# Performance work log

Hardware: AMD Instinct MI355X
Metric: run time of the kernel (lower is better)

The kernel has to match this reference:

```python
import jax, jax.numpy as jnp
import numpy as np
import math

H, Dh, S = 8, 64, 3          # heads, dim per head, samples factor
B, T, N, K = 2, 12, 512, 16  # batch, time, nodes, local-adj width
F = H * Dh                   # features = 512
SN = int(S * math.log2(N))   # Sampled_Nodes = 27
EPS = 1e-5


def setup_inputs() -> dict:
    key = jax.random.key(0)
    ks = jax.random.split(key, 22)
    sc = 1.0 / math.sqrt(F)
    W = lambda k: jax.random.normal(k, (F, F), jnp.float32) * sc
    bb = lambda k: jax.random.normal(k, (F,), jnp.float32) * 0.01
    return {
        "x": jax.random.normal(ks[0], (B, T, N, F), jnp.float32),
        "spa_eigvalue": jax.random.normal(ks[1], (F,), jnp.float32) * 0.1,
        "spa_eigvec": jax.random.normal(ks[2], (N, F), jnp.float32) * 0.1,
        "tem_eigvalue": jax.random.normal(ks[3], (F,), jnp.float32) * 0.1,
        "tem_eigvec": jax.random.normal(ks[4], (N, F), jnp.float32) * 0.1,
        "localadj": jax.random.randint(ks[5], (N, K), 0, N),
        "Wq": W(ks[6]), "bq": bb(ks[7]),
        "Wk": W(ks[8]), "bk": bb(ks[9]),
        "Wv": W(ks[10]), "bv": bb(ks[11]),
        "Wo": W(ks[12]), "bo": bb(ks[13]),
        "w_proj": jax.random.normal(ks[14], (K,), jnp.float32) / math.sqrt(K),
        "b_proj": jax.random.normal(ks[15], (), jnp.float32) * 0.01,
        "gamma": jnp.ones((F,), jnp.float32),
        "beta": jnp.zeros((F,), jnp.float32),
        "W1": W(ks[16]), "b1": bb(ks[17]),
        "W2": W(ks[18]), "b2": bb(ks[19]),
    }


def _lin(v, Wm, bv):  # torch nn.Linear: y = x @ W^T + b, W is [out, in]
    return jnp.einsum('...i,oi->...o', v, Wm) + bv


def _ln(v, g=None, b=None):  # LayerNorm over last dim, eps=1e-5
    mu = jnp.mean(v, -1, keepdims=True)
    var = jnp.var(v, -1, keepdims=True)
    y = (v - mu) * jax.lax.rsqrt(var + EPS)
    return y * g + b if g is not None else y


def reference(x, spa_eigvalue, spa_eigvec, tem_eigvalue, tem_eigvec, localadj,
              Wq, bq, Wk, bk, Wv, bv, Wo, bo, w_proj, b_proj,
              gamma, beta, W1, b1, W2, b2):
    # eigvec @ diag(eigval) == row-wise scaling
    x_ = x + (spa_eigvec * spa_eigvalue + tem_eigvec * tem_eigvalue)
    to_heads = lambda v: v.reshape(B, T, N, H, Dh).transpose(3, 0, 1, 2, 4)  # [H,B,T,N,Dh]
    Qh = to_heads(_lin(x_, Wq, bq))
    Kh = to_heads(_lin(x_, Wk, bk))
    Vh = to_heads(_lin(x_, Wv, bv))
    # local-adjacency K sampling: [H,B,T,N,K,Dh]
    Ks = Kh[:, :, :, localadj, :]
    qks = jnp.einsum('hbtnd,hbtnkd->hbtnk', Qh, Ks)
    # importance score per query node via learned projection over K neighbors
    M = jnp.einsum('hbtnk,k->hbtn', qks, w_proj) + b_proj
    _, m_top = jax.lax.top_k(M, SN)                              # [H,B,T,SN]
    Qr = jnp.take_along_axis(Qh, m_top[..., None], axis=3)       # [H,B,T,SN,Dh]
    scores = jnp.einsum('hbtsd,hbtnd->hbtsn', Qr, Kh) / math.sqrt(Dh)
    attn = jax.nn.softmax(scores, axis=-1)                       # [H,B,T,SN,N]
    cp = jnp.argmax(attn, axis=-2)                               # best sampled query per key node [H,B,T,N]
    val = jnp.einsum('hbtsn,hbtnd->hbtsd', attn, Vh)             # [H,B,T,SN,Dh]
    out = jnp.take_along_axis(val, cp[..., None], axis=3)        # [H,B,T,N,Dh]
    out = out.transpose(1, 2, 3, 0, 4).reshape(B, T, N, F)       # merge heads
    v = _ln(_lin(out, Wo, bo), gamma, beta)
    h = jax.nn.relu(_lin(v, W1, b1))
    h = _lin(h, W2, b2) + v
    return _ln(h)
```

## Files before the change

### kernel.cpp

```cpp
#include <hip/hip_runtime.h>
#include <math.h>

#define H_    8
#define DH    64
#define NN    512
#define KADJ  16
#define FF    512
#define BTOT  24
#define ROWS  12288
#define SN_   27
#define EPS_  1e-5f

typedef short short8 __attribute__((ext_vector_type(8)));
typedef float f32x4  __attribute__((ext_vector_type(4)));

__device__ __forceinline__ ushort f2bf(float x) {
    uint u = __float_as_uint(x);
    u += 0x7FFFu + ((u >> 16) & 1u);
    return (ushort)(u >> 16);
}
__device__ __forceinline__ float bf2f(ushort h) {
    return __uint_as_float(((uint)h) << 16);
}
__device__ __forceinline__ void pack_hilo(float4 a, float4 b, short8& hi, short8& lo) {
    float v[8] = {a.x, a.y, a.z, a.w, b.x, b.y, b.z, b.w};
    #pragma unroll
    for (int j = 0; j < 8; ++j) {
        ushort h = f2bf(v[j]);
        hi[j] = (short)h;
        lo[j] = (short)f2bf(v[j] - bf2f(h));
    }
}

__device__ __forceinline__ void gload_lds16(const ushort* g, ushort* l) {
    __builtin_amdgcn_global_load_lds(
        (const __attribute__((address_space(1))) unsigned int*)g,
        (__attribute__((address_space(3))) unsigned int*)l,
        16, 0, 0);
}

__global__ __launch_bounds__(256) void add_pos_bf16(
    const float* __restrict__ x,
    const float* __restrict__ spa_val, const float* __restrict__ spa_vec,
    const float* __restrict__ tem_val, const float* __restrict__ tem_vec,
    ushort* __restrict__ xh, ushort* __restrict__ xl)
{
    int i = blockIdx.x * 256 + threadIdx.x;
    int f4  = i & 127;
    int row = i >> 7;
    int n   = row & (NN - 1);

    float4 xv = reinterpret_cast<const float4*>(x)[i];
    float4 sv = reinterpret_cast<const float4*>(spa_vec)[n * 128 + f4];
    float4 tv = reinterpret_cast<const float4*>(tem_vec)[n * 128 + f4];
    float4 se = reinterpret_cast<const float4*>(spa_val)[f4];
    float4 te = reinterpret_cast<const float4*>(tem_val)[f4];
    float r0 = xv.x + sv.x * se.x + tv.x * te.x;
    float r1 = xv.y + sv.y * se.y + tv.y * te.y;
    float r2 = xv.z + sv.z * se.z + tv.z * te.z;
    float r3 = xv.w + sv.w * se.w + tv.w * te.w;
    ushort h0 = f2bf(r0), h1 = f2bf(r1), h2 = f2bf(r2), h3 = f2bf(r3);
    reinterpret_cast<ushort4*>(xh)[i] = make_ushort4(h0, h1, h2, h3);
    reinterpret_cast<ushort4*>(xl)[i] = make_ushort4(
        f2bf(r0 - bf2f(h0)), f2bf(r1 - bf2f(h1)),
        f2bf(r2 - bf2f(h2)), f2bf(r3 - bf2f(h3)));
}

__global__ __launch_bounds__(256) void wconv_kernel(
    const float* __restrict__ w0, const float* __restrict__ w1,
    const float* __restrict__ w2, const float* __restrict__ w3,
    const float* __restrict__ w4, const float* __restrict__ w5,
    ushort* __restrict__ whi, ushort* __restrict__ wlo)
{
    const int wi = blockIdx.y;
    const float* W = wi == 0 ? w0 : wi == 1 ? w1 : wi == 2 ? w2 :
                     wi == 3 ? w3 : wi == 4 ? w4 : w5;
    int i = blockIdx.x * 256 + threadIdx.x;
    float4 v = reinterpret_cast<const float4*>(W)[i];
    ushort h0 = f2bf(v.x), h1 = f2bf(v.y), h2 = f2bf(v.z), h3 = f2bf(v.w);
    reinterpret_cast<ushort4*>(whi + (size_t)wi * 262144)[i] =
        make_ushort4(h0, h1, h2, h3);
    if (wi < 2) {
        reinterpret_cast<ushort4*>(wlo + (size_t)wi * 262144)[i] =
            make_ushort4(f2bf(v.x - bf2f(h0)), f2bf(v.y - bf2f(h1)),
                         f2bf(v.z - bf2f(h2)), f2bf(v.w - bf2f(h3)));
    }
}

#define GBM 64
#define GBN 128

template <int SPLIT, int EPI, int OUTBF>
__global__ __launch_bounds__(256, 2) void gemm_mfma2(
    const ushort* __restrict__ Ah, const ushort* __restrict__ Al,
    const ushort* __restrict__ Wh, const ushort* __restrict__ Wl,
    const float* __restrict__ bias, const float* __restrict__ addsrc,
    float* __restrict__ Cf, ushort* __restrict__ Cb)
{
    __shared__ ushort sA[GBM * 64];
    __shared__ ushort sB[GBN * 64];

    const int nx  = gridDim.x >> 3;
    const int bid = blockIdx.x;
    const int lt  = (bid & 7) * nx + (bid >> 3);
    const int rowBase = (lt >> 2) * GBM;
    const int colBase = (lt & 3) * GBN;

    const int tid  = threadIdx.x;
    const int lane = tid & 63;
    const int wid  = tid >> 6;
    const int q    = lane >> 4;
    const int fr   = lane & 15;
    const int wm   = wid & 1;
    const int wn   = wid >> 1;

    const int kadv = SPLIT ? 32 : 64;
    const ushort* asrc[2];
    const ushort* bsrc[4];
    #pragma unroll
    for (int c = 0; c < 2; ++c) {
        const int p   = wid * 2048 + c * 1024 + lane * 16;
        const int row = p >> 7;
        const int ss  = ((p >> 4) & 7) ^ (row & 7);
        if (!SPLIT)
            asrc[c] = Ah + (size_t)(rowBase + row) * FF + ss * 8;
        else
            asrc[c] = (ss < 4)
                ? Ah + (size_t)(rowBase + row) * FF + ss * 8
                : Al + (size_t)(rowBase + row) * FF + (ss - 4) * 8;
    }
    #pragma unroll
    for (int c = 0; c < 4; ++c) {
        const int p   = wid * 4096 + c * 1024 + lane * 16;
        const int row = p >> 7;
        const int ss  = ((p >> 4) & 7) ^ (row & 7);
        if (!SPLIT)
            bsrc[c] = Wh + (size_t)(colBase + row) * FF + ss * 8;
        else
            bsrc[c] = (ss < 4)
                ? Wh + (size_t)(colBase + row) * FF + ss * 8
                : Wl + (size_t)(colBase + row) * FF + (ss - 4) * 8;
    }

    f32x4 acc[2][4];
    #pragma unroll
    for (int mi = 0; mi < 2; ++mi)
        #pragma unroll
        for (int ni = 0; ni < 4; ++ni) acc[mi][ni] = (f32x4){0.f, 0.f, 0.f, 0.f};

    const int NSTEP = SPLIT ? 16 : 8;
    const int swz = fr & 7;

    for (int step = 0; step < NSTEP; ++step) {
        #pragma unroll
        for (int c = 0; c < 2; ++c) {
            gload_lds16(asrc[c], &sA[wid * 1024 + c * 512]);
            asrc[c] += kadv;
        }
        #pragma unroll
        for (int c = 0; c < 4; ++c) {
            gload_lds16(bsrc[c], &sB[wid * 2048 + c * 512]);
            bsrc[c] += kadv;
        }
        __syncthreads();

        if (!SPLIT) {
            #pragma unroll
            for (int ksub = 0; ksub < 2; ++ksub) {
                const int kq = ksub * 4 + q;
                short8 af[2], bf[4];
                #pragma unroll
                for (int mi = 0; mi < 2; ++mi)
                    af[mi] = *(const short8*)&sA[(wm * 32 + mi * 16 + fr) * 64 +
                                                 ((kq ^ swz) << 3)];
                #pragma unroll
                for (int ni = 0; ni < 4; ++ni)
                    bf[ni] = *(const short8*)&sB[(wn * 64 + ni * 16 + fr) * 64 +
                                                 ((kq ^ swz) << 3)];
                #pragma unroll
                for (int mi = 0; mi < 2; ++mi)
                    #pragma unroll
                    for (int ni = 0; ni < 4; ++ni)
                        acc[mi][ni] = __builtin_amdgcn_mfma_f32_16x16x32_bf16(
                            af[mi], bf[ni], acc[mi][ni], 0, 0, 0);
            }
        } else {
            short8 ah[2], bh[4], t[4];
            #pragma unroll
            for (int mi = 0; mi < 2; ++mi)
                ah[mi] = *(const short8*)&sA[(wm * 32 + mi * 16 + fr) * 64 +
                                             ((q ^ swz) << 3)];
            #pragma unroll
            for (int ni = 0; ni < 4; ++ni)
                bh[ni] = *(const short8*)&sB[(wn * 64 + ni * 16 + fr) * 64 +
                                             ((q ^ swz) << 3)];
            #pragma unroll
            for (int mi = 0; mi < 2; ++mi)
                #pragma unroll
                for (int ni = 0; ni < 4; ++ni)
                    acc[mi][ni] = __builtin_amdgcn_mfma_f32_16x16x32_bf16(
                        ah[mi], bh[ni], acc[mi][ni], 0, 0, 0);
            #pragma unroll
            for (int ni = 0; ni < 4; ++ni)
                t[ni] = *(const short8*)&sB[(wn * 64 + ni * 16 + fr) * 64 +
                                            (((q + 4) ^ swz) << 3)];
            #pragma unroll
            for (int mi = 0; mi < 2; ++mi)
                #pragma unroll
                for (int ni = 0; ni < 4; ++ni)
                    acc[mi][ni] = __builtin_amdgcn_mfma_f32_16x16x32_bf16(
                        ah[mi], t[ni], acc[mi][ni], 0, 0, 0);
            #pragma unroll
            for (int mi = 0; mi < 2; ++mi)
                t[mi] = *(const short8*)&sA[(wm * 32 + mi * 16 + fr) * 64 +
                                            (((q + 4) ^ swz) << 3)];
            #pragma unroll
            for (int mi = 0; mi < 2; ++mi)
                #pragma unroll
                for (int ni = 0; ni < 4; ++ni)
                    acc[mi][ni] = __builtin_amdgcn_mfma_f32_16x16x32_bf16(
                        t[mi], bh[ni], acc[mi][ni], 0, 0, 0);
        }
        __syncthreads();
    }

    #pragma unroll
    for (int mi = 0; mi < 2; ++mi)
        #pragma unroll
        for (int ni = 0; ni < 4; ++ni) {
            const int col = colBase + wn * 64 + ni * 16 + fr;
            const float bcol = bias[col];
            #pragma unroll
            for (int r = 0; r < 4; ++r) {
                const int row = rowBase + wm * 32 + mi * 16 + q * 4 + r;
                float v = acc[mi][ni][r] + bcol;
                if (EPI == 1) v = fmaxf(v, 0.0f);
                if (EPI == 2) v += addsrc[(size_t)row * FF + col];
                if (OUTBF) Cb[(size_t)row * FF + col] = f2bf(v);
                else       Cf[(size_t)row * FF + col] = v;
            }
        }
}

__global__ __launch_bounds__(256) void qks_M_kernel(
    const float* __restrict__ Q, const float* __restrict__ K,
    const int* __restrict__ adj, const float* __restrict__ w_proj,
    const float* __restrict__ b_proj, float* __restrict__ Mout)
{
    const int w = blockIdx.x * 4 + (threadIdx.x >> 6);
    const int lane = threadIdx.x & 63;
    const int n   = w & (NN - 1);
    const int hbt = w >> 9;
    const int h   = hbt / BTOT;
    const int bt  = hbt % BTOT;

    float s = 0.0f;
    #pragma unroll
    for (int k = 0; k < KADJ; ++k) {
        const int j = adj[n * KADJ + k];
        s += w_proj[k] * K[((size_t)(bt * NN + j)) * FF + h * DH + lane];
    }
    float t = Q[((size_t)(bt * NN + n)) * FF + h * DH + lane] * s;
    #pragma unroll
    for (int o = 32; o; o >>= 1) t += __shfl_xor(t, o);
    if (lane == 0) Mout[(size_t)hbt * NN + n] = t + b_proj[0];
}

__global__ __launch_bounds__(64) void topk_kernel(
    const float* __restrict__ M, int* __restrict__ mtop)
{
    const int g = blockIdx.x;
    __shared__ float vals[NN];
    const int lane = threadIdx.x;
    for (int i = lane; i < NN; i += 64) vals[i] = M[(size_t)g * NN + i];
    __syncthreads();

    for (int s = 0; s < SN_; ++s) {
        float bv = -INFINITY;
        int bi = 1 << 30;
        for (int i = lane; i < NN; i += 64) {
            float v = vals[i];
            if (v > bv || (v == bv && i < bi)) { bv = v; bi = i; }
        }
        #pragma unroll
        for (int o = 32; o; o >>= 1) {
            float ov = __shfl_xor(bv, o);
            int   oi = __shfl_xor(bi, o);
            if (ov > bv || (ov == bv && oi < bi)) { bv = ov; bi = oi; }
        }
        if (lane == 0) {
            mtop[g * SN_ + s] = bi;
            vals[bi] = -INFINITY;
        }
        __syncthreads();
    }
}

__global__ __launch_bounds__(512) void fused_attn(
    const float* __restrict__ Q, const float* __restrict__ K,
    const float* __restrict__ V, const int* __restrict__ mtop,
    ushort* __restrict__ attnout)
{
    __shared__ ushort P_lds[32 * 512];
    __shared__ ushort Vt_lds[64 * 512];
    __shared__ float red0[8][32];
    __shared__ float red1[8][32];
    __shared__ float val_lds[32][68];
    __shared__ int   cp_lds[NN];
    __shared__ int   mt[32];

    const int g = blockIdx.x;
    const int h = g / BTOT, bt = g % BTOT;
    const int tid = threadIdx.x;
    const int wave = tid >> 6, lane = tid & 63;
    const int q = lane >> 4, c = lane & 15;
    const size_t base_bt = (size_t)bt * NN * FF;
    const int hcol = h * DH;

    if (tid < 32) mt[tid] = mtop[g * SN_ + (tid < SN_ ? tid : 0)];

    float4 vreg[4][4];
    #pragma unroll
    for (int i = 0; i < 4; ++i) {
        const int u  = tid + i * 512;
        const int d4 = u & 15, ng = u >> 4;
        const float* vp = V + base_bt + (size_t)(ng * 4) * FF + hcol + d4 * 4;
        #pragma unroll
        for (int ii = 0; ii < 4; ++ii)
            vreg[i][ii] = *(const float4*)(vp + (size_t)ii * FF);
    }
    __syncthreads();

    short8 afh[2][2], afl[2][2];
    #pragma unroll
    for (int m = 0; m < 2; ++m) {
        const int grow = mt[m * 16 + c];
        const float* qp = Q + base_bt + (size_t)grow * FF + hcol + q * 8;
        #pragma unroll
        for (int ks = 0; ks < 2; ++ks) {
            float4 a0 = *(const float4*)(qp + ks * 32);
            float4 a1 = *(const float4*)(qp + ks * 32 + 4);
            pack_hilo(a0, a1, afh[m][ks], afl[m][ks]);
        }
    }

    const int n0 = wave * 64;
    short8 bfh[4][2], bfl[4][2];
    #pragma unroll
    for (int nt = 0; nt < 4; ++nt) {
        const int krow = n0 + nt * 16 + c;
        const float* kp = K + base_bt + (size_t)krow * FF + hcol + q * 8;
        #pragma unroll
        for (int ks = 0; ks < 2; ++ks) {
            float4 b0 = *(const float4*)(kp + ks * 32);
            float4 b1 = *(const float4*)(kp + ks * 32 + 4);
            pack_hilo(b0, b1, bfh[nt][ks], bfl[nt][ks]);
        }
    }

    f32x4 sc[2][4];
    #pragma unroll
    for (int m = 0; m < 2; ++m)
        #pragma unroll
        for (int nt = 0; nt < 4; ++nt) sc[m][nt] = (f32x4){0.f, 0.f, 0.f, 0.f};
    #pragma unroll
    for (int ks = 0; ks < 2; ++ks)
        #pragma unroll
        for (int m = 0; m < 2; ++m)
            #pragma unroll
            for (int nt = 0; nt < 4; ++nt) {
                sc[m][nt] = __builtin_amdgcn_mfma_f32_16x16x32_bf16(
                    afh[m][ks], bfh[nt][ks], sc[m][nt], 0, 0, 0);
                sc[m][nt] = __builtin_amdgcn_mfma_f32_16x16x32_bf16(
                    afh[m][ks], bfl[nt][ks], sc[m][nt], 0, 0, 0);
                sc[m][nt] = __builtin_amdgcn_mfma_f32_16x16x32_bf16(
                    afl[m][ks], bfh[nt][ks], sc[m][nt], 0, 0, 0);
            }
    #pragma unroll
    for (int m = 0; m < 2; ++m)
        #pragma unroll
        for (int nt = 0; nt < 4; ++nt)
            #pragma unroll
            for (int r = 0; r < 4; ++r) sc[m][nt][r] *= 0.125f;

    float rmax[2][4];
    #pragma unroll
    for (int m = 0; m < 2; ++m)
        #pragma unroll
        for (int r = 0; r < 4; ++r) {
            float v = sc[m][0][r];
            v = fmaxf(v, sc[m][1][r]);
            v = fmaxf(v, sc[m][2][r]);
            v = fmaxf(v, sc[m][3][r]);
            rmax[m][r] = v;
        }
    #pragma unroll
    for (int off = 1; off <= 8; off <<= 1)
        #pragma unroll
        for (int m = 0; m < 2; ++m)
            #pragma unroll
            for (int r = 0; r < 4; ++r)
                rmax[m][r] = fmaxf(rmax[m][r], __shfl_xor(rmax[m][r], off));
    if (c == 0) {
        #pragma unroll
        for (int m = 0; m < 2; ++m)
            #pragma unroll
            for (int r = 0; r < 4; ++r)
                red0[wave][m * 16 + q * 4 + r] = rmax[m][r];
    }
    __syncthreads();
    float gmax[2][4];
    #pragma unroll
    for (int m = 0; m < 2; ++m)
        #pragma unroll
        for (int r = 0; r < 4; ++r) {
            const int row = m * 16 + q * 4 + r;
            float v = red0[0][row];
            #pragma unroll
            for (int w = 1; w < 8; ++w) v = fmaxf(v, red0[w][row]);
            gmax[m][r] = v;
        }

    float rsum[2][4] = {};
    #pragma unroll
    for (int m = 0; m < 2; ++m)
        #pragma unroll
        for (int nt = 0; nt < 4; ++nt)
            #pragma unroll
            for (int r = 0; r < 4; ++r) {
                float e = expf(sc[m][nt][r] - gmax[m][r]);
                sc[m][nt][r] = e;
                rsum[m][r] += e;
            }
    #pragma unroll
    for (int off = 1; off <= 8; off <<= 1)
        #pragma unroll
        for (int m = 0; m < 2; ++m)
            #pragma unroll
            for (int r = 0; r < 4; ++r)
                rsum[m][r] += __shfl_xor(rsum[m][r], off);
    if (c == 0) {
        #pragma unroll
        for (int m = 0; m < 2; ++m)
            #pragma unroll
            for (int r = 0; r < 4; ++r)
                red1[wave][m * 16 + q * 4 + r] = rsum[m][r];
    }
    __syncthreads();
    #pragma unroll
    for (int m = 0; m < 2; ++m)
        #pragma unroll
        for (int r = 0; r < 4; ++r) {
            const int row = m * 16 + q * 4 + r;
            float s = red1[0][row];
            #pragma unroll
            for (int w = 1; w < 8; ++w) s += red1[w][row];
            const float inv = 1.0f / s;
            #pragma unroll
            for (int nt = 0; nt < 4; ++nt) sc[m][nt][r] *= inv;
        }

    #pragma unroll
    for (int nt = 0; nt < 4; ++nt) {
        float bv = -INFINITY;
        int bi = 1 << 30;
        #pragma unroll
        for (int m = 0; m < 2; ++m)
            #pragma unroll
            for (int r = 0; r < 4; ++r) {
                const int row = m * 16 + q * 4 + r;
                if (row < SN_) {
                    float v = sc[m][nt][r];
                    if (v > bv) { bv = v; bi = row; }
                }
            }
        #pragma unroll
        for (int off = 16; off <= 32; off <<= 1) {
            float ov = __shfl_xor(bv, off);
            int   oi = __shfl_xor(bi, off);
            if (ov > bv || (ov == bv && oi < bi)) { bv = ov; bi = oi; }
        }
        if (q == 0) cp_lds[n0 + nt * 16 + c] = bi;
    }

    #pragma unroll
    for (int m = 0; m < 2; ++m)
        #pragma unroll
        for (int nt = 0; nt < 4; ++nt)
            #pragma unroll
            for (int r = 0; r < 4; ++r) {
                const int row = m * 16 + q * 4 + r;
                const int col = n0 + nt * 16 + c;
                P_lds[(row * 512 + col) ^ ((row & 7) << 3)] = f2bf(sc[m][nt][r]);
            }

    #pragma unroll
    for (int i = 0; i < 4; ++i) {
        const int u  = tid + i * 512;
        const int d4 = u & 15, ng = u >> 4;
        const int n0v = ng * 4;
        #pragma unroll
        for (int j = 0; j < 4; ++j) {
            const int d = d4 * 4 + j;
            ushort4 t;
            t.x = f2bf(((const float*)&vreg[i][0])[j]);
            t.y = f2bf(((const float*)&vreg[i][1])[j]);
            t.z = f2bf(((const float*)&vreg[i][2])[j]);
            t.w = f2bf(((const float*)&vreg[i][3])[j]);
            const int addr = (d * 512 + n0v) ^ ((d & 7) << 3);
            *(ushort4*)&Vt_lds[addr] = t;
        }
    }
    __syncthreads();

    const int msel = wave >> 2, dt = wave & 3;
    const int dcol = dt * 16 + c;
    const int prow = msel * 16 + c;
    const int pswz = (prow & 7) << 3;
    const int vswz = (dcol & 7) << 3;
    f32x4 acc = (f32x4){0.f, 0.f, 0.f, 0.f};
    for (int kstep = 0; kstep < 16; ++kstep) {
        short8 a = *(const short8*)&P_lds[(prow * 512 + kstep * 32 + q * 8) ^ pswz];
        short8 b = *(const short8*)&Vt_lds[(dcol * 512 + kstep * 32 + q * 8) ^ vswz];
        acc = __builtin_amdgcn_mfma_f32_16x16x32_bf16(a, b, acc, 0, 0, 0);
    }
    #pragma unroll
    for (int r = 0; r < 4; ++r)
        val_lds[msel * 16 + q * 4 + r][dt * 16 + c] = acc[r];
    __syncthreads();

    #pragma unroll
    for (int pass = 0; pass < 8; ++pass) {
        const int n  = pass * 64 + (tid >> 3);
        const int s  = cp_lds[n];
        const int d0 = (tid & 7) * 8;
        const float* vr = &val_lds[s][d0];
        uint4 u;
        u.x = (uint)f2bf(vr[0]) | ((uint)f2bf(vr[1]) << 16);
        u.y = (uint)f2bf(vr[2]) | ((uint)f2bf(vr[3]) << 16);
        u.z = (uint)f2bf(vr[4]) | ((uint)f2bf(vr[5]) << 16);
        u.w = (uint)f2bf(vr[6]) | ((uint)f2bf(vr[7]) << 16);
        *(uint4*)(attnout + base_bt + (size_t)n * FF + hcol + d0) = u;
    }
}

template <int AFFINE, int BFOUT>
__global__ __launch_bounds__(256) void ln_kernel(
    const float* __restrict__ X, const float* __restrict__ g,
    const float* __restrict__ b, float* __restrict__ Yf,
    ushort* __restrict__ Yb, int rows)
{
    const int row = blockIdx.x * 4 + (threadIdx.x >> 6);
    if (row >= rows) return;
    const int lane = threadIdx.x & 63;
    const float4* x4 = reinterpret_cast<const float4*>(X + (size_t)row * FF);
    float4 a = x4[lane];
    float4 c = x4[lane + 64];
    float s = a.x + a.y + a.z + a.w + c.x + c.y + c.z + c.w;
    float q = a.x * a.x + a.y * a.y + a.z * a.z + a.w * a.w +
              c.x * c.x + c.y * c.y + c.z * c.z + c.w * c.w;
    #pragma unroll
    for (int o = 32; o; o >>= 1) {
        s += __shfl_xor(s, o);
        q += __shfl_xor(q, o);
    }
    const float mu   = s * (1.0f / FF);
    const float var  = q * (1.0f / FF) - mu * mu;
    const float rstd = 1.0f / sqrtf(var + EPS_);

    float4 ya, yc;
    ya.x = (a.x - mu) * rstd; ya.y = (a.y - mu) * rstd;
    ya.z = (a.z - mu) * rstd; ya.w = (a.w - mu) * rstd;
    yc.x = (c.x - mu) * rstd; yc.y = (c.y - mu) * rstd;
    yc.z = (c.z - mu) * rstd; yc.w = (c.w - mu) * rstd;
    if (AFFINE) {
        float4 ga = reinterpret_cast<const float4*>(g)[lane];
        float4 gc = reinterpret_cast<const float4*>(g)[lane + 64];
        float4 ba = reinterpret_cast<const float4*>(b)[lane];
        float4 bc = reinterpret_cast<const float4*>(b)[lane + 64];
        ya.x = ya.x * ga.x + ba.x; ya.y = ya.y * ga.y + ba.y;
        ya.z = ya.z * ga.z + ba.z; ya.w = ya.w * ga.w + ba.w;
        yc.x = yc.x * gc.x + bc.x; yc.y = yc.y * gc.y + bc.y;
        yc.z = yc.z * gc.z + bc.z; yc.w = yc.w * gc.w + bc.w;
    }
    float4* y4 = reinterpret_cast<float4*>(Yf + (size_t)row * FF);
    y4[lane]      = ya;
    y4[lane + 64] = yc;
    if (BFOUT) {
        ushort4* yb = reinterpret_cast<ushort4*>(Yb + (size_t)row * FF);
        yb[lane] = make_ushort4(f2bf(ya.x), f2bf(ya.y), f2bf(ya.z), f2bf(ya.w));
        yb[lane + 64] = make_ushort4(f2bf(yc.x), f2bf(yc.y), f2bf(yc.z), f2bf(yc.w));
    }
}

extern "C" void kernel_launch(void* const* d_in, const int* in_sizes, int n_in,
                              void* d_out, int out_size, void* d_ws, size_t ws_size,
                              hipStream_t stream)
{
    const float* x       = (const float*)d_in[0];
    const float* spa_val = (const float*)d_in[1];
    const float* spa_vec = (const float*)d_in[2];
    const float* tem_val = (const float*)d_in[3];
    const float* tem_vec = (const float*)d_in[4];
    const int*   adj     = (const int*)  d_in[5];
    const float* Wq = (const float*)d_in[6];  const float* bq = (const float*)d_in[7];
    const float* Wk = (const float*)d_in[8];  const float* bk = (const float*)d_in[9];
    const float* Wv = (const float*)d_in[10]; const float* bv = (const float*)d_in[11];
    const float* Wo = (const float*)d_in[12]; const float* bo = (const float*)d_in[13];
    const float* w_proj = (const float*)d_in[14];
    const float* b_proj = (const float*)d_in[15];
    const float* gamma  = (const float*)d_in[16];
    const float* beta   = (const float*)d_in[17];
    const float* W1 = (const float*)d_in[18]; const float* b1 = (const float*)d_in[19];
    const float* W2 = (const float*)d_in[20]; const float* b2 = (const float*)d_in[21];

    float* out = (float*)d_out;
    float* ws  = (float*)d_ws;

    const size_t R = (size_t)ROWS * FF;

    float* bufQ = ws;
    float* bufK = ws + R;
    float* bufV = ws + 2 * R;
    ushort* whi = (ushort*)(ws + 3 * R);
    ushort* wlo = whi + 6 * 262144;
    float* Mbuf = ws + 3 * R + (6 * 262144 + 2 * 262144) / 2;
    int*   mtop = (int*)(Mbuf + (size_t)H_ * BTOT * NN);

    ushort* xh  = (ushort*)d_out;
    ushort* xl  = xh + R;
    ushort* attnout = xh;
    ushort* vbf = xl;
    ushort* h1b = xh;

    add_pos_bf16<<<(ROWS * FF / 4) / 256, 256, 0, stream>>>(
        x, spa_val, spa_vec, tem_val, tem_vec, xh, xl);

    wconv_kernel<<<dim3(256, 6), 256, 0, stream>>>(Wq, Wk, Wv, Wo, W1, W2, whi, wlo);

    const int NG = (ROWS / GBM) * (FF / GBN);
    gemm_mfma2<1, 0, 0><<<NG, 256, 0, stream>>>(xh, xl, whi, wlo, bq, nullptr, bufQ, nullptr);
    gemm_mfma2<1, 0, 0><<<NG, 256, 0, stream>>>(xh, xl, whi + 262144, wlo + 262144, bk, nullptr, bufK, nullptr);
    gemm_mfma2<0, 0, 0><<<NG, 256, 0, stream>>>(xh, nullptr, whi + 2 * 262144, nullptr, bv, nullptr, bufV, nullptr);

    qks_M_kernel<<<(H_ * BTOT * NN) / 4, 256, 0, stream>>>(
        bufQ, bufK, adj, w_proj, b_proj, Mbuf);
    topk_kernel<<<H_ * BTOT, 64, 0, stream>>>(Mbuf, mtop);

    fused_attn<<<H_ * BTOT, 512, 0, stream>>>(bufQ, bufK, bufV, mtop, attnout);

    gemm_mfma2<0, 0, 0><<<NG, 256, 0, stream>>>(attnout, nullptr, whi + 3 * 262144, nullptr, bo, nullptr, bufQ, nullptr);
    ln_kernel<1, 1><<<ROWS / 4, 256, 0, stream>>>(bufQ, gamma, beta, bufK, vbf, ROWS);
    gemm_mfma2<0, 1, 1><<<NG, 256, 0, stream>>>(vbf, nullptr, whi + 4 * 262144, nullptr, b1, nullptr, nullptr, h1b);
    gemm_mfma2<0, 2, 0><<<NG, 256, 0, stream>>>(h1b, nullptr, whi + 5 * 262144, nullptr, b2, bufK, bufV, nullptr);
    ln_kernel<0, 0><<<ROWS / 4, 256, 0, stream>>>(bufV, nullptr, nullptr, out, nullptr, ROWS);
}
```

Before: 234.9 us.

## Store Q/K as bf16 hi/lo pairs, V as bf16; widen attention to 1024 threads

```diff
diff --git a/kernel.cpp b/kernel.cpp
--- a/kernel.cpp
+++ b/kernel.cpp
@@ -21,15 +21,6 @@
 }
 __device__ __forceinline__ float bf2f(ushort h) {
     return __uint_as_float(((uint)h) << 16);
-}
-__device__ __forceinline__ void pack_hilo(float4 a, float4 b, short8& hi, short8& lo) {
-    float v[8] = {a.x, a.y, a.z, a.w, b.x, b.y, b.z, b.w};
-    #pragma unroll
-    for (int j = 0; j < 8; ++j) {
-        ushort h = f2bf(v[j]);
-        hi[j] = (short)h;
-        lo[j] = (short)f2bf(v[j] - bf2f(h));
-    }
 }
 
 __device__ __forceinline__ void gload_lds16(const ushort* g, ushort* l) {
@@ -90,12 +81,12 @@
 #define GBM 64
 #define GBN 128
 
-template <int SPLIT, int EPI, int OUTBF>
+template <int SPLIT, int EPI, int OUT>
 __global__ __launch_bounds__(256, 2) void gemm_mfma2(
     const ushort* __restrict__ Ah, const ushort* __restrict__ Al,
     const ushort* __restrict__ Wh, const ushort* __restrict__ Wl,
     const float* __restrict__ bias, const float* __restrict__ addsrc,
-    float* __restrict__ Cf, ushort* __restrict__ Cb)
+    float* __restrict__ Cf, ushort* __restrict__ Cb, ushort* __restrict__ Cl)
 {
     __shared__ ushort sA[GBM * 64];
     __shared__ ushort sB[GBN * 64];
@@ -236,14 +227,21 @@
                 float v = acc[mi][ni][r] + bcol;
                 if (EPI == 1) v = fmaxf(v, 0.0f);
                 if (EPI == 2) v += addsrc[(size_t)row * FF + col];
-                if (OUTBF) Cb[(size_t)row * FF + col] = f2bf(v);
-                else       Cf[(size_t)row * FF + col] = v;
+                const size_t idx = (size_t)row * FF + col;
+                if (OUT == 0) Cf[idx] = v;
+                if (OUT == 1) Cb[idx] = f2bf(v);
+                if (OUT == 2) {
+                    ushort hh = f2bf(v);
+                    Cb[idx] = hh;
+                    Cl[idx] = f2bf(v - bf2f(hh));
+                }
             }
         }
 }
 
 __global__ __launch_bounds__(256) void qks_M_kernel(
-    const float* __restrict__ Q, const float* __restrict__ K,
+    const ushort* __restrict__ Qh, const ushort* __restrict__ Ql,
+    const ushort* __restrict__ Kh, const ushort* __restrict__ Kl,
     const int* __restrict__ adj, const float* __restrict__ w_proj,
     const float* __restrict__ b_proj, float* __restrict__ Mout)
 {
@@ -258,9 +256,11 @@
     #pragma unroll
     for (int k = 0; k < KADJ; ++k) {
         const int j = adj[n * KADJ + k];
-        s += w_proj[k] * K[((size_t)(bt * NN + j)) * FF + h * DH + lane];
-    }
-    float t = Q[((size_t)(bt * NN + n)) * FF + h * DH + lane] * s;
+        const size_t idx = ((size_t)(bt * NN + j)) * FF + h * DH + lane;
+        s += w_proj[k] * (bf2f(Kh[idx]) + bf2f(Kl[idx]));
+    }
+    const size_t qidx = ((size_t)(bt * NN + n)) * FF + h * DH + lane;
+    float t = (bf2f(Qh[qidx]) + bf2f(Ql[qidx])) * s;
     #pragma unroll
     for (int o = 32; o; o >>= 1) t += __shfl_xor(t, o);
     if (lane == 0) Mout[(size_t)hbt * NN + n] = t + b_proj[0];
@@ -296,16 +296,17 @@
     }
 }
 
-__global__ __launch_bounds__(512) void fused_attn(
-    const float* __restrict__ Q, const float* __restrict__ K,
-    const float* __restrict__ V, const int* __restrict__ mtop,
+__global__ __launch_bounds__(1024) void fused_attn(
+    const ushort* __restrict__ Qh, const ushort* __restrict__ Ql,
+    const ushort* __restrict__ Kh, const ushort* __restrict__ Kl,
+    const ushort* __restrict__ Vb, const int* __restrict__ mtop,
     ushort* __restrict__ attnout)
 {
     __shared__ ushort P_lds[32 * 512];
     __shared__ ushort Vt_lds[64 * 512];
-    __shared__ float red0[8][32];
-    __shared__ float red1[8][32];
-    __shared__ float val_lds[32][68];
+    __shared__ float red0[16][32];
+    __shared__ float red1[16][32];
+    __shared__ float val2[2][32][68];
     __shared__ int   cp_lds[NN];
     __shared__ int   mt[32];
 
@@ -318,57 +319,54 @@
     const int hcol = h * DH;
 
     if (tid < 32) mt[tid] = mtop[g * SN_ + (tid < SN_ ? tid : 0)];
-
-    float4 vreg[4][4];
-    #pragma unroll
-    for (int i = 0; i < 4; ++i) {
-        const int u  = tid + i * 512;
+    __syncthreads();
+
+    const int n0 = wave * 32;
+    short8 bfh[2][2], bfl[2][2];
+    #pragma unroll
+    for (int nt = 0; nt < 2; ++nt) {
+        const size_t kp = base_bt + (size_t)(n0 + nt * 16 + c) * FF + hcol + q * 8;
+        #pragma unroll
+        for (int ks = 0; ks < 2; ++ks) {
+            bfh[nt][ks] = *(const short8*)&Kh[kp + ks * 32];
+            bfl[nt][ks] = *(const short8*)&Kl[kp + ks * 32];
+        }
+    }
+
+    ushort4 vreg[2][4];
+    #pragma unroll
+    for (int i = 0; i < 2; ++i) {
+        const int u  = tid + i * 1024;
         const int d4 = u & 15, ng = u >> 4;
-        const float* vp = V + base_bt + (size_t)(ng * 4) * FF + hcol + d4 * 4;
         #pragma unroll
         for (int ii = 0; ii < 4; ++ii)
-            vreg[i][ii] = *(const float4*)(vp + (size_t)ii * FF);
-    }
-    __syncthreads();
+            vreg[i][ii] = *(const ushort4*)&Vb[base_bt +
+                (size_t)(ng * 4 + ii) * FF + hcol + d4 * 4];
+    }
 
     short8 afh[2][2], afl[2][2];
     #pragma unroll
     for (int m = 0; m < 2; ++m) {
         const int grow = mt[m * 16 + c];
-        const float* qp = Q + base_bt + (size_t)grow * FF + hcol + q * 8;
+        const size_t qp = base_bt + (size_t)grow * FF + hcol + q * 8;
         #pragma unroll
         for (int ks = 0; ks < 2; ++ks) {
-            float4 a0 = *(const float4*)(qp + ks * 32);
-            float4 a1 = *(const float4*)(qp + ks * 32 + 4);
-            pack_hilo(a0, a1, afh[m][ks], afl[m][ks]);
-        }
-    }
-
-    const int n0 = wave * 64;
-    short8 bfh[4][2], bfl[4][2];
-    #pragma unroll
-    for (int nt = 0; nt < 4; ++nt) {
-        const int krow = n0 + nt * 16 + c;
-        const float* kp = K + base_bt + (size_t)krow * FF + hcol + q * 8;
-        #pragma unroll
-        for (int ks = 0; ks < 2; ++ks) {
-            float4 b0 = *(const float4*)(kp + ks * 32);
-            float4 b1 = *(const float4*)(kp + ks * 32 + 4);
-            pack_hilo(b0, b1, bfh[nt][ks], bfl[nt][ks]);
-        }
-    }
-
-    f32x4 sc[2][4];
+            afh[m][ks] = *(const short8*)&Qh[qp + ks * 32];
+            afl[m][ks] = *(const short8*)&Ql[qp + ks * 32];
+        }
+    }
+
+    f32x4 sc[2][2];
     #pragma unroll
     for (int m = 0; m < 2; ++m)
         #pragma unroll
-        for (int nt = 0; nt < 4; ++nt) sc[m][nt] = (f32x4){0.f, 0.f, 0.f, 0.f};
+        for (int nt = 0; nt < 2; ++nt) sc[m][nt] = (f32x4){0.f, 0.f, 0.f, 0.f};
     #pragma unroll
     for (int ks = 0; ks < 2; ++ks)
         #pragma unroll
         for (int m = 0; m < 2; ++m)
             #pragma unroll
-            for (int nt = 0; nt < 4; ++nt) {
+            for (int nt = 0; nt < 2; ++nt) {
                 sc[m][nt] = __builtin_amdgcn_mfma_f32_16x16x32_bf16(
                     afh[m][ks], bfh[nt][ks], sc[m][nt], 0, 0, 0);
                 sc[m][nt] = __builtin_amdgcn_mfma_f32_16x16x32_bf16(
@@ -379,7 +377,7 @@
     #pragma unroll
     for (int m = 0; m < 2; ++m)
         #pragma unroll
-        for (int nt = 0; nt < 4; ++nt)
+        for (int nt = 0; nt < 2; ++nt)
             #pragma unroll
             for (int r = 0; r < 4; ++r) sc[m][nt][r] *= 0.125f;
 
@@ -387,13 +385,8 @@
     #pragma unroll
     for (int m = 0; m < 2; ++m)
         #pragma unroll
-        for (int r = 0; r < 4; ++r) {
-            float v = sc[m][0][r];
-            v = fmaxf(v, sc[m][1][r]);
-            v = fmaxf(v, sc[m][2][r]);
-            v = fmaxf(v, sc[m][3][r]);
-            rmax[m][r] = v;
-        }
+        for (int r = 0; r < 4; ++r)
+            rmax[m][r] = fmaxf(sc[m][0][r], sc[m][1][r]);
     #pragma unroll
     for (int off = 1; off <= 8; off <<= 1)
         #pragma unroll
@@ -417,7 +410,7 @@
             const int row = m * 16 + q * 4 + r;
             float v = red0[0][row];
             #pragma unroll
-            for (int w = 1; w < 8; ++w) v = fmaxf(v, red0[w][row]);
+            for (int w = 1; w < 16; ++w) v = fmaxf(v, red0[w][row]);
             gmax[m][r] = v;
         }
 
@@ -425,7 +418,7 @@
     #pragma unroll
     for (int m = 0; m < 2; ++m)
         #pragma unroll
-        for (int nt = 0; nt < 4; ++nt)
+        for (int nt = 0; nt < 2; ++nt)
             #pragma unroll
             for (int r = 0; r < 4; ++r) {
                 float e = expf(sc[m][nt][r] - gmax[m][r]);
@@ -454,14 +447,14 @@
             const int row = m * 16 + q * 4 + r;
             float s = red1[0][row];
             #pragma unroll
-            for (int w = 1; w < 8; ++w) s += red1[w][row];
+            for (int w = 1; w < 16; ++w) s += red1[w][row];
             const float inv = 1.0f / s;
             #pragma unroll
-            for (int nt = 0; nt < 4; ++nt) sc[m][nt][r] *= inv;
-        }
-
-    #pragma unroll
-    for (int nt = 0; nt < 4; ++nt) {
+            for (int nt = 0; nt < 2; ++nt) sc[m][nt][r] *= inv;
+        }
+
+    #pragma unroll
+    for (int nt = 0; nt < 2; ++nt) {
         float bv = -INFINITY;
         int bi = 1 << 30;
         #pragma unroll
@@ -486,7 +479,7 @@
     #pragma unroll
     for (int m = 0; m < 2; ++m)
         #pragma unroll
-        for (int nt = 0; nt < 4; ++nt)
+        for (int nt = 0; nt < 2; ++nt)
             #pragma unroll
             for (int r = 0; r < 4; ++r) {
                 const int row = m * 16 + q * 4 + r;
@@ -495,46 +488,51 @@
             }
 
     #pragma unroll
-    for (int i = 0; i < 4; ++i) {
-        const int u  = tid + i * 512;
+    for (int i = 0; i < 2; ++i) {
+        const int u  = tid + i * 1024;
         const int d4 = u & 15, ng = u >> 4;
         const int n0v = ng * 4;
         #pragma unroll
         for (int j = 0; j < 4; ++j) {
             const int d = d4 * 4 + j;
             ushort4 t;
-            t.x = f2bf(((const float*)&vreg[i][0])[j]);
-            t.y = f2bf(((const float*)&vreg[i][1])[j]);
-            t.z = f2bf(((const float*)&vreg[i][2])[j]);
-            t.w = f2bf(((const float*)&vreg[i][3])[j]);
-            const int addr = (d * 512 + n0v) ^ ((d & 7) << 3);
-            *(ushort4*)&Vt_lds[addr] = t;
+            t.x = ((const ushort*)&vreg[i][0])[j];
+            t.y = ((const ushort*)&vreg[i][1])[j];
+            t.z = ((const ushort*)&vreg[i][2])[j];
+            t.w = ((const ushort*)&vreg[i][3])[j];
+            *(ushort4*)&Vt_lds[(d * 512 + n0v) ^ ((d & 7) << 3)] = t;
         }
     }
     __syncthreads();
 
-    const int msel = wave >> 2, dt = wave & 3;
+    const int kh = wave >> 3, rem = wave & 7;
+    const int msel = rem >> 2, dt = rem & 3;
     const int dcol = dt * 16 + c;
     const int prow = msel * 16 + c;
     const int pswz = (prow & 7) << 3;
     const int vswz = (dcol & 7) << 3;
     f32x4 acc = (f32x4){0.f, 0.f, 0.f, 0.f};
-    for (int kstep = 0; kstep < 16; ++kstep) {
+    #pragma unroll
+    for (int ks8 = 0; ks8 < 8; ++ks8) {
+        const int kstep = kh * 8 + ks8;
         short8 a = *(const short8*)&P_lds[(prow * 512 + kstep * 32 + q * 8) ^ pswz];
         short8 b = *(const short8*)&Vt_lds[(dcol * 512 + kstep * 32 + q * 8) ^ vswz];
         acc = __builtin_amdgcn_mfma_f32_16x16x32_bf16(a, b, acc, 0, 0, 0);
     }
     #pragma unroll
     for (int r = 0; r < 4; ++r)
-        val_lds[msel * 16 + q * 4 + r][dt * 16 + c] = acc[r];
+        val2[kh][msel * 16 + q * 4 + r][dt * 16 + c] = acc[r];
     __syncthreads();
 
     #pragma unroll
-    for (int pass = 0; pass < 8; ++pass) {
-        const int n  = pass * 64 + (tid >> 3);
+    for (int pass = 0; pass < 4; ++pass) {
+        const int n  = pass * 128 + (tid >> 3);
         const int s  = cp_lds[n];
         const int d0 = (tid & 7) * 8;
-        const float* vr = &val_lds[s][d0];
+        float vr[8];
+        #pragma unroll
+        for (int j = 0; j < 8; ++j)
+            vr[j] = val2[0][s][d0 + j] + val2[1][s][d0 + j];
         uint4 u;
         u.x = (uint)f2bf(vr[0]) | ((uint)f2bf(vr[1]) << 16);
         u.y = (uint)f2bf(vr[2]) | ((uint)f2bf(vr[3]) << 16);
@@ -615,17 +613,23 @@
     const float* W2 = (const float*)d_in[20]; const float* b2 = (const float*)d_in[21];
 
     float* out = (float*)d_out;
-    float* ws  = (float*)d_ws;
 
     const size_t R = (size_t)ROWS * FF;
 
-    float* bufQ = ws;
-    float* bufK = ws + R;
-    float* bufV = ws + 2 * R;
-    ushort* whi = (ushort*)(ws + 3 * R);
-    ushort* wlo = whi + 6 * 262144;
-    float* Mbuf = ws + 3 * R + (6 * 262144 + 2 * 262144) / 2;
-    int*   mtop = (int*)(Mbuf + (size_t)H_ * BTOT * NN);
+    ushort* ws_u = (ushort*)d_ws;
+    ushort* bufQh = ws_u;
+    ushort* bufQl = ws_u + R;
+    ushort* bufKh = ws_u + 2 * R;
+    ushort* bufKl = ws_u + 3 * R;
+    ushort* bufVb = ws_u + 4 * R;
+    ushort* whi   = ws_u + 5 * R;
+    ushort* wlo   = whi + 6 * 262144;
+    float*  Mbuf  = (float*)(wlo + 2 * 262144);
+    int*    mtop  = (int*)(Mbuf + (size_t)H_ * BTOT * NN);
+
+    float* o_f32 = (float*)bufQh;
+    float* v_f32 = (float*)bufKh;
+    float* h2_f32 = (float*)bufQh;
 
     ushort* xh  = (ushort*)d_out;
     ushort* xl  = xh + R;
@@ -639,19 +643,26 @@
     wconv_kernel<<<dim3(256, 6), 256, 0, stream>>>(Wq, Wk, Wv, Wo, W1, W2, whi, wlo);
 
     const int NG = (ROWS / GBM) * (FF / GBN);
-    gemm_mfma2<1, 0, 0><<<NG, 256, 0, stream>>>(xh, xl, whi, wlo, bq, nullptr, bufQ, nullptr);
-    gemm_mfma2<1, 0, 0><<<NG, 256, 0, stream>>>(xh, xl, whi + 262144, wlo + 262144, bk, nullptr, bufK, nullptr);
-    gemm_mfma2<0, 0, 0><<<NG, 256, 0, stream>>>(xh, nullptr, whi + 2 * 262144, nullptr, bv, nullptr, bufV, nullptr);
+    gemm_mfma2<1, 0, 2><<<NG, 256, 0, stream>>>(xh, xl, whi, wlo, bq, nullptr,
+                                                nullptr, bufQh, bufQl);
+    gemm_mfma2<1, 0, 2><<<NG, 256, 0, stream>>>(xh, xl, whi + 262144, wlo + 262144,
+                                                bk, nullptr, nullptr, bufKh, bufKl);
+    gemm_mfma2<0, 0, 1><<<NG, 256, 0, stream>>>(xh, nullptr, whi + 2 * 262144, nullptr,
+                                                bv, nullptr, nullptr, bufVb, nullptr);
 
     qks_M_kernel<<<(H_ * BTOT * NN) / 4, 256, 0, stream>>>(
-        bufQ, bufK, adj, w_proj, b_proj, Mbuf);
+        bufQh, bufQl, bufKh, bufKl, adj, w_proj, b_proj, Mbuf);
     topk_kernel<<<H_ * BTOT, 64, 0, stream>>>(Mbuf, mtop);
 
-    fused_attn<<<H_ * BTOT, 512, 0, stream>>>(bufQ, bufK, bufV, mtop, attnout);
-
-    gemm_mfma2<0, 0, 0><<<NG, 256, 0, stream>>>(attnout, nullptr, whi + 3 * 262144, nullptr, bo, nullptr, bufQ, nullptr);
-    ln_kernel<1, 1><<<ROWS / 4, 256, 0, stream>>>(bufQ, gamma, beta, bufK, vbf, ROWS);
-    gemm_mfma2<0, 1, 1><<<NG, 256, 0, stream>>>(vbf, nullptr, whi + 4 * 262144, nullptr, b1, nullptr, nullptr, h1b);
-    gemm_mfma2<0, 2, 0><<<NG, 256, 0, stream>>>(h1b, nullptr, whi + 5 * 262144, nullptr, b2, bufK, bufV, nullptr);
-    ln_kernel<0, 0><<<ROWS / 4, 256, 0, stream>>>(bufV, nullptr, nullptr, out, nullptr, ROWS);
-}
+    fused_attn<<<H_ * BTOT, 1024, 0, stream>>>(
+        bufQh, bufQl, bufKh, bufKl, bufVb, mtop, attnout);
+
+    gemm_mfma2<0, 0, 0><<<NG, 256, 0, stream>>>(attnout, nullptr, whi + 3 * 262144,
+                                                nullptr, bo, nullptr, o_f32, nullptr, nullptr);
+    ln_kernel<1, 1><<<ROWS / 4, 256, 0, stream>>>(o_f32, gamma, beta, v_f32, vbf, ROWS);
+    gemm_mfma2<0, 1, 1><<<NG, 256, 0, stream>>>(vbf, nullptr, whi + 4 * 262144, nullptr,
+                                                b1, nullptr, nullptr, h1b, nullptr);
+    gemm_mfma2<0, 2, 0><<<NG, 256, 0, stream>>>(h1b, nullptr, whi + 5 * 262144, nullptr,
+                                                b2, v_f32, h2_f32, nullptr, nullptr);
+    ln_kernel<0, 0><<<ROWS / 4, 256, 0, stream>>>(h2_f32, nullptr, nullptr, out, nullptr, ROWS);
+}
```

Measured after the change: 248.1 us. +5.6%, slower.
